# Kernel optimization log

Hardware: AMD Instinct MI355X
Metric: run time of the kernel (lower is better)

The kernel has to match this reference:

```python
import jax, jax.numpy as jnp
import numpy as np

TAU = 0.05
ALPHA = 0.5
LARGE_NUM = 1.0e9
EPS = 1e-12  # F.normalize eps


def setup_inputs() -> dict:
    key = jax.random.key(0)
    k1, k2 = jax.random.split(key)
    emb = jax.random.normal(k1, (200000, 128), dtype=jnp.float32)
    train_links = jax.random.randint(k2, (4096, 2), 0, 200000, dtype=jnp.int64)
    return {"emb": emb, "train_links": train_links}


def reference(emb, train_links):
    # L2-normalize rows (torch F.normalize with eps clamp)
    norm = jnp.maximum(jnp.linalg.norm(emb, axis=1, keepdims=True), EPS)
    embn = emb / norm

    zis = embn[train_links[:, 0]]  # [B, d]
    zjs = embn[train_links[:, 1]]  # [B, d]
    B = zis.shape[0]

    mask = jnp.eye(B, dtype=zis.dtype) * LARGE_NUM  # self-similarity mask

    logits_aa = zis @ zis.T / TAU - mask            # [B, B]
    logits_bb = zjs @ zjs.T / TAU - mask            # [B, B]
    logits_ab = zis @ zjs.T / TAU                   # [B, B]
    logits_ba = zjs @ zis.T / TAU                   # [B, B]

    logits_a = jnp.concatenate([logits_ab, logits_aa], axis=1)  # [B, 2B]
    logits_b = jnp.concatenate([logits_ba, logits_bb], axis=1)  # [B, 2B]

    # labels are one-hot at column i (diagonal of the ab/ba block):
    # softXEnt = -(one_hot * log_softmax).sum() / B = -mean(diag log-prob)
    idx = jnp.arange(B)
    logp_a = jax.nn.log_softmax(logits_a, axis=1)
    logp_b = jax.nn.log_softmax(logits_b, axis=1)
    loss_a = -jnp.mean(logp_a[idx, idx])
    loss_b = -jnp.mean(logp_b[idx, idx])

    return ALPHA * loss_a + (1.0 - ALPHA) * loss_b
```

## Files before the change

### kernel.cpp

```cpp
#include <hip/hip_runtime.h>
#include <hip/hip_bf16.h>
#include <math.h>

typedef __attribute__((ext_vector_type(8))) short short8;
typedef __attribute__((ext_vector_type(16))) float f32x16;

#define NB 4096
#define DIM 128
#define SQS 5.3715828f

#if __has_builtin(__builtin_amdgcn_exp2f)
#define EX2(x) __builtin_amdgcn_exp2f(x)
#else
#define EX2(x) exp2f(x)
#endif

__device__ inline unsigned short f2bf(float f) {
  unsigned int u = __builtin_bit_cast(unsigned int, f);
  u += 0x7FFFu + ((u >> 16) & 1u);
  return (unsigned short)(u >> 16);
}

__device__ inline float wave_sum(float v) {
#pragma unroll
  for (int off = 32; off >= 1; off >>= 1) v += __shfl_xor(v, off, 64);
  return v;
}

__global__ __launch_bounds__(64) void k_init(const int* links32, int* flag, float* out) {
  int t = threadIdx.x;
  bool ok = (links32[1 + 2 * t] == 0) && (links32[129 + 2 * t] == 0);
  unsigned long long m = __ballot(ok);
  if (t == 0) { *flag = (m == ~0ull) ? 1 : 0; out[0] = 0.0f; }
}

__global__ __launch_bounds__(256) void k_normalize(
    const float* __restrict__ emb, const int* __restrict__ links,
    const int* __restrict__ flag,
    unsigned short* __restrict__ Zic, unsigned short* __restrict__ Zjc,
    float* __restrict__ diagn) {
  int wid = threadIdx.x >> 6, lane = threadIdx.x & 63;
  int p = blockIdx.x * 4 + wid;
  int fl = *flag;
  int idx_i = fl ? links[4 * p + 0] : links[2 * p + 0];
  int idx_j = fl ? links[4 * p + 2] : links[2 * p + 1];
  const float* si = emb + (long long)idx_i * DIM;
  const float* sj = emb + (long long)idx_j * DIM;
  float a0 = si[lane], a1 = si[lane + 64];
  float b0 = sj[lane], b1 = sj[lane + 64];
  float sii = wave_sum(a0 * a0 + a1 * a1);
  float sjj = wave_sum(b0 * b0 + b1 * b1);
  float sij = wave_sum(a0 * b0 + a1 * b1);
  float ni = fmaxf(sqrtf(sii), 1e-12f);
  float nj = fmaxf(sqrtf(sjj), 1e-12f);
  if (lane == 0) diagn[p] = 20.0f * sij / (ni * nj);
  float wi = SQS / ni, wj = SQS / nj;
  size_t o0 = (((size_t)(lane >> 3) + 0) * NB + p) * 8 + (lane & 7);
  size_t o1 = (((size_t)(lane >> 3) + 8) * NB + p) * 8 + (lane & 7);
  Zic[o0] = f2bf(a0 * wi);
  Zic[o1] = f2bf(a1 * wi);
  Zjc[o0] = f2bf(b0 * wj);
  Zjc[o1] = f2bf(b1 * wj);
}

__global__ __launch_bounds__(256, 2) void k_pass(
    const unsigned short* __restrict__ Zic, const unsigned short* __restrict__ Zjc,
    float* __restrict__ rowp_a, float* __restrict__ rowp_b) {
  __shared__ unsigned short yt[2][2][4096];
  __shared__ float bufa[128], bufb[128];
  int tid = threadIdx.x, wid = tid >> 6, lane = tid & 63;
  if (tid < 128) { bufa[tid] = 0.0f; bufb[tid] = 0.0f; }

  int it0 = blockIdx.x * 128 + wid * 32;
  int jb = blockIdx.y * 256;
  int lr = lane & 31;
  int hi = lane >> 5;

  short8 pj, pc;
  unsigned short blr = f2bf((float)lr);
#pragma unroll
  for (int e = 0; e < 8; ++e) { pj[e] = (short)blr; pc[e] = (short)0x3D80; }
  f32x16 pr = {}, pn = {};
  pr = __builtin_amdgcn_mfma_f32_32x32x16_bf16(pj, pc, pr, 0, 0, 0);
  pn = __builtin_amdgcn_mfma_f32_32x32x16_bf16(pc, pj, pn, 0, 0, 0);
  unsigned int dmask = 0;
  int imv[4] = {0, 0, 0, 0};
#pragma unroll
  for (int r = 0; r < 16; ++r) {
    int jm = (int)(pr[r] + 0.5f), im = (int)(pn[r] + 0.5f);
    dmask |= (unsigned)(jm == im) << r;
    imv[r >> 2] |= im << ((r & 3) * 8);
  }

  short8 xi[8], xj[8];
#pragma unroll
  for (int ks = 0; ks < 8; ++ks) {
    size_t o = ((size_t)(ks * 2 + hi) * NB + (it0 + lr)) * 8;
    xi[ks] = *reinterpret_cast<const short8*>(Zic + o);
    xj[ks] = *reinterpret_cast<const short8*>(Zjc + o);
  }

  float ra[16], rb[16];
#pragma unroll
  for (int r = 0; r < 16; ++r) { ra[r] = 0.0f; rb[r] = 0.0f; }

#pragma unroll
  for (int q = 0; q < 2; ++q) {
    int p = q * 256 + tid;
    size_t go = ((size_t)(p >> 5) * NB + (jb + (p & 31))) * 8;
    *reinterpret_cast<short8*>(&yt[0][0][p * 8]) =
        *reinterpret_cast<const short8*>(Zjc + go);
    *reinterpret_cast<short8*>(&yt[0][1][p * 8]) =
        *reinterpret_cast<const short8*>(Zic + go);
  }
  __syncthreads();

  for (int jt = 0; jt < 8; ++jt) {
    int cur = jt & 1, nxt = cur ^ 1;
    int j0 = jb + jt * 32;
    bool dt = (j0 == it0);
    short8 tj0, ti0, tj1, ti1;
    if (jt < 7) {
      int j0n = j0 + 32;
      size_t g0 = ((size_t)(tid >> 5) * NB + (j0n + (tid & 31))) * 8;
      size_t g1 = ((size_t)((tid + 256) >> 5) * NB + (j0n + (tid & 31))) * 8;
      tj0 = *reinterpret_cast<const short8*>(Zjc + g0);
      ti0 = *reinterpret_cast<const short8*>(Zic + g0);
      tj1 = *reinterpret_cast<const short8*>(Zjc + g1);
      ti1 = *reinterpret_cast<const short8*>(Zic + g1);
    }
    f32x16 pab = {}, pbb = {}, paa = {}, pba = {};
#pragma unroll
    for (int ks = 0; ks < 8; ++ks) {
      int off = ((ks * 2 + hi) * 32 + lr) * 8;
      short8 yj = *reinterpret_cast<const short8*>(&yt[cur][0][off]);
      short8 yi = *reinterpret_cast<const short8*>(&yt[cur][1][off]);
      pab = __builtin_amdgcn_mfma_f32_32x32x16_bf16(yj, xi[ks], pab, 0, 0, 0);
      pbb = __builtin_amdgcn_mfma_f32_32x32x16_bf16(yj, xj[ks], pbb, 0, 0, 0);
      paa = __builtin_amdgcn_mfma_f32_32x32x16_bf16(yi, xi[ks], paa, 0, 0, 0);
      pba = __builtin_amdgcn_mfma_f32_32x32x16_bf16(yi, xj[ks], pba, 0, 0, 0);
    }
    if (jt < 7) {
      *reinterpret_cast<short8*>(&yt[nxt][0][tid * 8]) = tj0;
      *reinterpret_cast<short8*>(&yt[nxt][1][tid * 8]) = ti0;
      *reinterpret_cast<short8*>(&yt[nxt][0][(tid + 256) * 8]) = tj1;
      *reinterpret_cast<short8*>(&yt[nxt][1][(tid + 256) * 8]) = ti1;
    }
#pragma unroll
    for (int r = 0; r < 16; ++r) {
      float eab = EX2(pab[r]);
      float ebb = EX2(pbb[r]);
      float eaa = EX2(paa[r]);
      float eba = EX2(pba[r]);
      if (dt && ((dmask >> r) & 1u)) { ebb = 0.0f; eaa = 0.0f; }
      ra[r] += eab + eaa;
      rb[r] += ebb + eba;
    }
    __syncthreads();
  }
#pragma unroll
  for (int r = 0; r < 16; ++r) {
    int im = (imv[r >> 2] >> ((r & 3) * 8)) & 0xFF;
    atomicAdd(&bufa[wid * 32 + im], ra[r]);
    atomicAdd(&bufb[wid * 32 + im], rb[r]);
  }
  __syncthreads();
  if (tid < 128) {
    rowp_a[(size_t)blockIdx.y * NB + blockIdx.x * 128 + tid] = bufa[tid];
    rowp_b[(size_t)blockIdx.y * NB + blockIdx.x * 128 + tid] = bufb[tid];
  }
}

__global__ __launch_bounds__(256) void k_final(
    const float* __restrict__ rowp_a, const float* __restrict__ rowp_b,
    const float* __restrict__ diagn, float* __restrict__ out) {
  int i = blockIdx.x * 256 + threadIdx.x;
  float sa = 0.0f, sb = 0.0f;
#pragma unroll
  for (int y = 0; y < 16; ++y) {
    sa += rowp_a[(size_t)y * NB + i];
    sb += rowp_b[(size_t)y * NB + i];
  }
  float v = 0.5f * (logf(sa) + logf(sb)) - diagn[i];
  v = wave_sum(v);
  __shared__ float sred[4];
  if ((threadIdx.x & 63) == 0) sred[threadIdx.x >> 6] = v;
  __syncthreads();
  if (threadIdx.x == 0)
    atomicAdd(out, (sred[0] + sred[1] + sred[2] + sred[3]) * (1.0f / NB));
}

extern "C" void kernel_launch(void* const* d_in, const int* in_sizes, int n_in,
                              void* d_out, int out_size, void* d_ws, size_t ws_size,
                              hipStream_t stream) {
  const float* emb = (const float*)d_in[0];
  const int* links = (const int*)d_in[1];
  char* ws = (char*)d_ws;
  unsigned short* Zic = (unsigned short*)(ws + 0);
  unsigned short* Zjc = (unsigned short*)(ws + 1048576);
  float* rowp_a = (float*)(ws + 2097152);
  float* rowp_b = (float*)(ws + 2359296);
  float* diagn = (float*)(ws + 2621440);
  int* flag = (int*)(ws + 2637824);
  float* out = (float*)d_out;

  hipLaunchKernelGGL(k_init, dim3(1), dim3(64), 0, stream, links, flag, out);
  hipLaunchKernelGGL(k_normalize, dim3(1024), dim3(256), 0, stream,
                     emb, links, flag, Zic, Zjc, diagn);
  hipLaunchKernelGGL(k_pass, dim3(32, 16), dim3(256), 0, stream,
                     Zic, Zjc, rowp_a, rowp_b);
  hipLaunchKernelGGL(k_final, dim3(16), dim3(256), 0, stream,
                     rowp_a, rowp_b, diagn, out);
}
```

Before: 54.29 us.

## Split column range finer, preload whole tile to LDS, reduce partials atomically

The pass kernel now covers 128 columns per block instead of 256, which doubles the grid to 32x32 blocks. Each block loads its entire column tile (both Zi and Zj, 64KB) into shared memory once, replacing the double-buffered prefetch loop with its per-iteration barriers. Per-row partial sums are accumulated with global atomics into a single zeroed buffer, so the final kernel no longer sums 16 partials; this needs an extra zeroing kernel. The larger LDS footprint and the removed occupancy hint may lower resident blocks per CU, and the up-front load is no longer overlapped with compute.

```diff
diff --git a/kernel.cpp b/kernel.cpp
--- a/kernel.cpp
+++ b/kernel.cpp
@@ -63,18 +63,27 @@
   Zjc[o1] = f2bf(b1 * wj);
 }
 
-__global__ __launch_bounds__(256, 2) void k_pass(
+__global__ __launch_bounds__(256) void k_pass(
     const unsigned short* __restrict__ Zic, const unsigned short* __restrict__ Zjc,
     float* __restrict__ rowp_a, float* __restrict__ rowp_b) {
-  __shared__ unsigned short yt[2][2][4096];
+  __shared__ unsigned short yt[2][16][128][8];
   __shared__ float bufa[128], bufb[128];
   int tid = threadIdx.x, wid = tid >> 6, lane = tid & 63;
   if (tid < 128) { bufa[tid] = 0.0f; bufb[tid] = 0.0f; }
 
   int it0 = blockIdx.x * 128 + wid * 32;
-  int jb = blockIdx.y * 256;
+  int jb = blockIdx.y * 128;
   int lr = lane & 31;
   int hi = lane >> 5;
+
+#pragma unroll
+  for (int q = 0; q < 16; ++q) {
+    int p = q * 256 + tid;
+    int s = p >> 11, c = (p >> 7) & 15, row = p & 127;
+    const unsigned short* Zs = s ? Zic : Zjc;
+    *reinterpret_cast<short8*>(&yt[s][c][row][0]) =
+        *reinterpret_cast<const short8*>(Zs + ((size_t)c * NB + jb + row) * 8);
+  }
 
   short8 pj, pc;
   unsigned short blr = f2bf((float)lr);
@@ -104,47 +113,20 @@
 #pragma unroll
   for (int r = 0; r < 16; ++r) { ra[r] = 0.0f; rb[r] = 0.0f; }
 
-#pragma unroll
-  for (int q = 0; q < 2; ++q) {
-    int p = q * 256 + tid;
-    size_t go = ((size_t)(p >> 5) * NB + (jb + (p & 31))) * 8;
-    *reinterpret_cast<short8*>(&yt[0][0][p * 8]) =
-        *reinterpret_cast<const short8*>(Zjc + go);
-    *reinterpret_cast<short8*>(&yt[0][1][p * 8]) =
-        *reinterpret_cast<const short8*>(Zic + go);
-  }
   __syncthreads();
 
-  for (int jt = 0; jt < 8; ++jt) {
-    int cur = jt & 1, nxt = cur ^ 1;
+  for (int jt = 0; jt < 4; ++jt) {
     int j0 = jb + jt * 32;
     bool dt = (j0 == it0);
-    short8 tj0, ti0, tj1, ti1;
-    if (jt < 7) {
-      int j0n = j0 + 32;
-      size_t g0 = ((size_t)(tid >> 5) * NB + (j0n + (tid & 31))) * 8;
-      size_t g1 = ((size_t)((tid + 256) >> 5) * NB + (j0n + (tid & 31))) * 8;
-      tj0 = *reinterpret_cast<const short8*>(Zjc + g0);
-      ti0 = *reinterpret_cast<const short8*>(Zic + g0);
-      tj1 = *reinterpret_cast<const short8*>(Zjc + g1);
-      ti1 = *reinterpret_cast<const short8*>(Zic + g1);
-    }
     f32x16 pab = {}, pbb = {}, paa = {}, pba = {};
 #pragma unroll
     for (int ks = 0; ks < 8; ++ks) {
-      int off = ((ks * 2 + hi) * 32 + lr) * 8;
-      short8 yj = *reinterpret_cast<const short8*>(&yt[cur][0][off]);
-      short8 yi = *reinterpret_cast<const short8*>(&yt[cur][1][off]);
+      short8 yj = *reinterpret_cast<const short8*>(&yt[0][ks * 2 + hi][jt * 32 + lr][0]);
+      short8 yi = *reinterpret_cast<const short8*>(&yt[1][ks * 2 + hi][jt * 32 + lr][0]);
       pab = __builtin_amdgcn_mfma_f32_32x32x16_bf16(yj, xi[ks], pab, 0, 0, 0);
       pbb = __builtin_amdgcn_mfma_f32_32x32x16_bf16(yj, xj[ks], pbb, 0, 0, 0);
       paa = __builtin_amdgcn_mfma_f32_32x32x16_bf16(yi, xi[ks], paa, 0, 0, 0);
       pba = __builtin_amdgcn_mfma_f32_32x32x16_bf16(yi, xj[ks], pba, 0, 0, 0);
-    }
-    if (jt < 7) {
-      *reinterpret_cast<short8*>(&yt[nxt][0][tid * 8]) = tj0;
-      *reinterpret_cast<short8*>(&yt[nxt][1][tid * 8]) = ti0;
-      *reinterpret_cast<short8*>(&yt[nxt][0][(tid + 256) * 8]) = tj1;
-      *reinterpret_cast<short8*>(&yt[nxt][1][(tid + 256) * 8]) = ti1;
     }
 #pragma unroll
     for (int r = 0; r < 16; ++r) {
@@ -156,7 +138,6 @@
       ra[r] += eab + eaa;
       rb[r] += ebb + eba;
     }
-    __syncthreads();
   }
 #pragma unroll
   for (int r = 0; r < 16; ++r) {
@@ -166,22 +147,21 @@
   }
   __syncthreads();
   if (tid < 128) {
-    rowp_a[(size_t)blockIdx.y * NB + blockIdx.x * 128 + tid] = bufa[tid];
-    rowp_b[(size_t)blockIdx.y * NB + blockIdx.x * 128 + tid] = bufb[tid];
+    atomicAdd(&rowp_a[blockIdx.x * 128 + tid], bufa[tid]);
+    atomicAdd(&rowp_b[blockIdx.x * 128 + tid], bufb[tid]);
   }
+}
+
+__global__ __launch_bounds__(256) void k_zero(float* rowp_a, float* rowp_b) {
+  int i = blockIdx.x * 256 + threadIdx.x;
+  if (i < NB) { rowp_a[i] = 0.0f; rowp_b[i] = 0.0f; }
 }
 
 __global__ __launch_bounds__(256) void k_final(
     const float* __restrict__ rowp_a, const float* __restrict__ rowp_b,
     const float* __restrict__ diagn, float* __restrict__ out) {
   int i = blockIdx.x * 256 + threadIdx.x;
-  float sa = 0.0f, sb = 0.0f;
-#pragma unroll
-  for (int y = 0; y < 16; ++y) {
-    sa += rowp_a[(size_t)y * NB + i];
-    sb += rowp_b[(size_t)y * NB + i];
-  }
-  float v = 0.5f * (logf(sa) + logf(sb)) - diagn[i];
+  float v = 0.5f * (logf(rowp_a[i]) + logf(rowp_b[i])) - diagn[i];
   v = wave_sum(v);
   __shared__ float sred[4];
   if ((threadIdx.x & 63) == 0) sred[threadIdx.x >> 6] = v;
@@ -199,15 +179,16 @@
   unsigned short* Zic = (unsigned short*)(ws + 0);
   unsigned short* Zjc = (unsigned short*)(ws + 1048576);
   float* rowp_a = (float*)(ws + 2097152);
-  float* rowp_b = (float*)(ws + 2359296);
-  float* diagn = (float*)(ws + 2621440);
-  int* flag = (int*)(ws + 2637824);
+  float* rowp_b = (float*)(ws + 2113536);
+  float* diagn = (float*)(ws + 2129920);
+  int* flag = (int*)(ws + 2146304);
   float* out = (float*)d_out;
 
   hipLaunchKernelGGL(k_init, dim3(1), dim3(64), 0, stream, links, flag, out);
+  hipLaunchKernelGGL(k_zero, dim3(16), dim3(256), 0, stream, rowp_a, rowp_b);
   hipLaunchKernelGGL(k_normalize, dim3(1024), dim3(256), 0, stream,
                      emb, links, flag, Zic, Zjc, diagn);
-  hipLaunchKernelGGL(k_pass, dim3(32, 16), dim3(256), 0, stream,
+  hipLaunchKernelGGL(k_pass, dim3(32, 32), dim3(256), 0, stream,
                      Zic, Zjc, rowp_a, rowp_b);
   hipLaunchKernelGGL(k_final, dim3(16), dim3(256), 0, stream,
                      rowp_a, rowp_b, diagn, out);
```

Result: slower. 78.21 us (+44.1%).

## Split contrastive pass by side via grid z to cut registers and raise occupancy

Applied to the files above, without the earlier changes.

Each k_pass block now computes only one side's row sums (a or b), selected by blockIdx.z. It keeps one set of query fragments and one accumulator instead of two sets and four MFMA accumulators. Launch bounds rise to 4 waves per SIMD and the grid doubles. This lowers register pressure so more waves can hide latency. In exchange, every key tile is loaded into shared memory twice, once by each side's block, and the total tile count rises.

```diff
diff --git a/kernel.cpp b/kernel.cpp
--- a/kernel.cpp
+++ b/kernel.cpp
@@ -7,6 +7,7 @@
 
 #define NB 4096
 #define DIM 128
+#define NJ 16
 #define SQS 5.3715828f
 
 #if __has_builtin(__builtin_amdgcn_exp2f)
@@ -63,16 +64,17 @@
   Zjc[o1] = f2bf(b1 * wj);
 }
 
-__global__ __launch_bounds__(256, 2) void k_pass(
+__global__ __launch_bounds__(256, 4) void k_pass(
     const unsigned short* __restrict__ Zic, const unsigned short* __restrict__ Zjc,
-    float* __restrict__ rowp_a, float* __restrict__ rowp_b) {
+    float* __restrict__ rowp) {
   __shared__ unsigned short yt[2][2][4096];
-  __shared__ float bufa[128], bufb[128];
+  __shared__ float bufr[128];
   int tid = threadIdx.x, wid = tid >> 6, lane = tid & 63;
-  if (tid < 128) { bufa[tid] = 0.0f; bufb[tid] = 0.0f; }
+  int side = blockIdx.z;
+  if (tid < 128) bufr[tid] = 0.0f;
 
   int it0 = blockIdx.x * 128 + wid * 32;
-  int jb = blockIdx.y * 256;
+  int jb = blockIdx.y * (NB / NJ);
   int lr = lane & 31;
   int hi = lane >> 5;
 
@@ -92,17 +94,16 @@
     imv[r >> 2] |= im << ((r & 3) * 8);
   }
 
-  short8 xi[8], xj[8];
-#pragma unroll
-  for (int ks = 0; ks < 8; ++ks) {
-    size_t o = ((size_t)(ks * 2 + hi) * NB + (it0 + lr)) * 8;
-    xi[ks] = *reinterpret_cast<const short8*>(Zic + o);
-    xj[ks] = *reinterpret_cast<const short8*>(Zjc + o);
-  }
-
-  float ra[16], rb[16];
-#pragma unroll
-  for (int r = 0; r < 16; ++r) { ra[r] = 0.0f; rb[r] = 0.0f; }
+  const unsigned short* Xs = side ? Zjc : Zic;
+  short8 x[8];
+#pragma unroll
+  for (int ks = 0; ks < 8; ++ks)
+    x[ks] = *reinterpret_cast<const short8*>(
+        Xs + ((size_t)(ks * 2 + hi) * NB + (it0 + lr)) * 8);
+
+  float rs[16];
+#pragma unroll
+  for (int r = 0; r < 16; ++r) rs[r] = 0.0f;
 
 #pragma unroll
   for (int q = 0; q < 2; ++q) {
@@ -129,57 +130,73 @@
       tj1 = *reinterpret_cast<const short8*>(Zjc + g1);
       ti1 = *reinterpret_cast<const short8*>(Zic + g1);
     }
-    f32x16 pab = {}, pbb = {}, paa = {}, pba = {};
-#pragma unroll
-    for (int ks = 0; ks < 8; ++ks) {
-      int off = ((ks * 2 + hi) * 32 + lr) * 8;
-      short8 yj = *reinterpret_cast<const short8*>(&yt[cur][0][off]);
-      short8 yi = *reinterpret_cast<const short8*>(&yt[cur][1][off]);
-      pab = __builtin_amdgcn_mfma_f32_32x32x16_bf16(yj, xi[ks], pab, 0, 0, 0);
-      pbb = __builtin_amdgcn_mfma_f32_32x32x16_bf16(yj, xj[ks], pbb, 0, 0, 0);
-      paa = __builtin_amdgcn_mfma_f32_32x32x16_bf16(yi, xi[ks], paa, 0, 0, 0);
-      pba = __builtin_amdgcn_mfma_f32_32x32x16_bf16(yi, xj[ks], pba, 0, 0, 0);
+    {
+      f32x16 a = {};
+#pragma unroll
+      for (int ks = 0; ks < 8; ++ks) {
+        int off = ((ks * 2 + hi) * 32 + lr) * 8;
+        short8 y = *reinterpret_cast<const short8*>(&yt[cur][0][off]);
+        a = __builtin_amdgcn_mfma_f32_32x32x16_bf16(y, x[ks], a, 0, 0, 0);
+      }
+      if (side && dt) {
+#pragma unroll
+        for (int r = 0; r < 16; ++r) {
+          float e = EX2(a[r]);
+          if ((dmask >> r) & 1u) e = 0.0f;
+          rs[r] += e;
+        }
+      } else {
+#pragma unroll
+        for (int r = 0; r < 16; ++r) rs[r] += EX2(a[r]);
+      }
     }
-    if (jt < 7) {
-      *reinterpret_cast<short8*>(&yt[nxt][0][tid * 8]) = tj0;
-      *reinterpret_cast<short8*>(&yt[nxt][1][tid * 8]) = ti0;
-      *reinterpret_cast<short8*>(&yt[nxt][0][(tid + 256) * 8]) = tj1;
-      *reinterpret_cast<short8*>(&yt[nxt][1][(tid + 256) * 8]) = ti1;
-    }
-#pragma unroll
-    for (int r = 0; r < 16; ++r) {
-      float eab = EX2(pab[r]);
-      float ebb = EX2(pbb[r]);
-      float eaa = EX2(paa[r]);
-      float eba = EX2(pba[r]);
-      if (dt && ((dmask >> r) & 1u)) { ebb = 0.0f; eaa = 0.0f; }
-      ra[r] += eab + eaa;
-      rb[r] += ebb + eba;
+    {
+      f32x16 a = {};
+#pragma unroll
+      for (int ks = 0; ks < 8; ++ks) {
+        int off = ((ks * 2 + hi) * 32 + lr) * 8;
+        short8 y = *reinterpret_cast<const short8*>(&yt[cur][1][off]);
+        a = __builtin_amdgcn_mfma_f32_32x32x16_bf16(y, x[ks], a, 0, 0, 0);
+      }
+      if (jt < 7) {
+        *reinterpret_cast<short8*>(&yt[nxt][0][tid * 8]) = tj0;
+        *reinterpret_cast<short8*>(&yt[nxt][1][tid * 8]) = ti0;
+        *reinterpret_cast<short8*>(&yt[nxt][0][(tid + 256) * 8]) = tj1;
+        *reinterpret_cast<short8*>(&yt[nxt][1][(tid + 256) * 8]) = ti1;
+      }
+      if (!side && dt) {
+#pragma unroll
+        for (int r = 0; r < 16; ++r) {
+          float e = EX2(a[r]);
+          if ((dmask >> r) & 1u) e = 0.0f;
+          rs[r] += e;
+        }
+      } else {
+#pragma unroll
+        for (int r = 0; r < 16; ++r) rs[r] += EX2(a[r]);
+      }
     }
     __syncthreads();
   }
 #pragma unroll
   for (int r = 0; r < 16; ++r) {
     int im = (imv[r >> 2] >> ((r & 3) * 8)) & 0xFF;
-    atomicAdd(&bufa[wid * 32 + im], ra[r]);
-    atomicAdd(&bufb[wid * 32 + im], rb[r]);
+    atomicAdd(&bufr[wid * 32 + im], rs[r]);
   }
   __syncthreads();
-  if (tid < 128) {
-    rowp_a[(size_t)blockIdx.y * NB + blockIdx.x * 128 + tid] = bufa[tid];
-    rowp_b[(size_t)blockIdx.y * NB + blockIdx.x * 128 + tid] = bufb[tid];
-  }
+  if (tid < 128)
+    rowp[((size_t)side * NJ + blockIdx.y) * NB + blockIdx.x * 128 + tid] = bufr[tid];
 }
 
 __global__ __launch_bounds__(256) void k_final(
-    const float* __restrict__ rowp_a, const float* __restrict__ rowp_b,
-    const float* __restrict__ diagn, float* __restrict__ out) {
+    const float* __restrict__ rowp, const float* __restrict__ diagn,
+    float* __restrict__ out) {
   int i = blockIdx.x * 256 + threadIdx.x;
   float sa = 0.0f, sb = 0.0f;
 #pragma unroll
-  for (int y = 0; y < 16; ++y) {
-    sa += rowp_a[(size_t)y * NB + i];
-    sb += rowp_b[(size_t)y * NB + i];
+  for (int y = 0; y < NJ; ++y) {
+    sa += rowp[(size_t)(0 * NJ + y) * NB + i];
+    sb += rowp[(size_t)(1 * NJ + y) * NB + i];
   }
   float v = 0.5f * (logf(sa) + logf(sb)) - diagn[i];
   v = wave_sum(v);
@@ -198,8 +215,7 @@
   char* ws = (char*)d_ws;
   unsigned short* Zic = (unsigned short*)(ws + 0);
   unsigned short* Zjc = (unsigned short*)(ws + 1048576);
-  float* rowp_a = (float*)(ws + 2097152);
-  float* rowp_b = (float*)(ws + 2359296);
+  float* rowp = (float*)(ws + 2097152);
   float* diagn = (float*)(ws + 2621440);
   int* flag = (int*)(ws + 2637824);
   float* out = (float*)d_out;
@@ -207,8 +223,8 @@
   hipLaunchKernelGGL(k_init, dim3(1), dim3(64), 0, stream, links, flag, out);
   hipLaunchKernelGGL(k_normalize, dim3(1024), dim3(256), 0, stream,
                      emb, links, flag, Zic, Zjc, diagn);
-  hipLaunchKernelGGL(k_pass, dim3(32, 16), dim3(256), 0, stream,
-                     Zic, Zjc, rowp_a, rowp_b);
+  hipLaunchKernelGGL(k_pass, dim3(32, NJ, 2), dim3(256), 0, stream,
+                     Zic, Zjc, rowp);
   hipLaunchKernelGGL(k_final, dim3(16), dim3(256), 0, stream,
-                     rowp_a, rowp_b, diagn, out);
-}
+                     rowp, diagn, out);
+}
```

New measurement: 54.94 us. No clear change (+1.2%).
